# Performance work log

Hardware: AMD Instinct MI355X
Metric: run time of the kernel (lower is better)

## Reference

```python
import jax, jax.numpy as jnp
import numpy as np

N_NODES = 100000
N_EDGES = 1600000
D_IN = 128
D_HID = 128
D_OUT = 16


def gcn_conv(x, W, b, src, dst, deg_inv_sqrt, deg_inv):
    # PyG GCNConv: transform then normalized aggregate with self-loops.
    h = x @ W  # [N, H]
    norm = deg_inv_sqrt[src] * deg_inv_sqrt[dst]  # [E]
    msg = h[src] * norm[:, None]  # [E, H] gather
    agg = jax.ops.segment_sum(msg, dst, num_segments=N_NODES)  # scatter-add
    agg = agg + h * deg_inv[:, None]  # self-loop term (weight deg^-1)
    return agg + b


def setup_inputs() -> dict:
    key = jax.random.key(0)
    ks = jax.random.split(key, 10)
    x = jax.random.normal(ks[0], (N_NODES, D_IN), dtype=jnp.float32)
    edge_index = jax.random.randint(ks[1], (2, N_EDGES), 0, N_NODES)
    s = 1.0 / np.sqrt(D_IN)
    sh = 1.0 / np.sqrt(D_HID)
    W0 = jax.random.uniform(ks[2], (D_IN, D_HID), jnp.float32, -s, s)
    b0 = jnp.zeros((D_HID,), jnp.float32)
    W1 = jax.random.uniform(ks[3], (D_HID, D_HID), jnp.float32, -sh, sh)
    b1 = jnp.zeros((D_HID,), jnp.float32)
    W2 = jax.random.uniform(ks[4], (D_HID, D_HID), jnp.float32, -sh, sh)
    b2 = jnp.zeros((D_HID,), jnp.float32)
    Wr = jax.random.uniform(ks[5], (D_HID, D_OUT), jnp.float32, -sh, sh)
    br = jax.random.uniform(ks[6], (D_OUT,), jnp.float32, -sh, sh)
    return {"x": x, "edge_index": edge_index, "W0": W0, "b0": b0,
            "W1": W1, "b1": b1, "W2": W2, "b2": b2, "Wr": Wr, "br": br}


def reference(x, edge_index, W0, b0, W1, b1, W2, b2, Wr, br):
    src, dst = edge_index[0], edge_index[1]
    # degree with self-loops: deg[i] = 1 + indegree(i)
    deg = jax.ops.segment_sum(jnp.ones((N_EDGES,), x.dtype), dst,
                              num_segments=N_NODES) + 1.0
    deg_inv_sqrt = deg ** -0.5
    deg_inv = 1.0 / deg
    h = x
    for W, b in ((W0, b0), (W1, b1), (W2, b2)):
        h = gcn_conv(h, W, b, src, dst, deg_inv_sqrt, deg_inv)
        h = jax.nn.relu(h)  # dropout is identity at inference
    out = h @ Wr + br
    return jax.nn.sigmoid(out) * 0.8 + 0.1
```

## Files before the change

### kernel.cpp

```cpp
#include <hip/hip_runtime.h>
#include <math.h>

#define N_NODES 100000
#define N_EDGES 1600000
#define NBUCKET 782
#define EB      256
#define EPB     6250

typedef __attribute__((ext_vector_type(8))) __bf16 bf16x8;
typedef __attribute__((ext_vector_type(4))) float  f32x4;


static __device__ __forceinline__ unsigned short f2bf(float f) {
    unsigned int u = __float_as_uint(f);
    unsigned int r = (u + 0x7FFFu + ((u >> 16) & 1u)) >> 16;
    return (unsigned short)r;
}
static __device__ __forceinline__ float bf2f(unsigned short h) {
    return __uint_as_float(((unsigned int)h) << 16);
}

__global__ void wconv_kernel(const float* __restrict__ W, unsigned short* __restrict__ Wt) {
    int n = blockIdx.x;
    int k = threadIdx.x;
    Wt[n * 128 + k] = f2bf(W[k * 128 + n]);
}


__global__ __launch_bounds__(256) void hist_kernel(const int* __restrict__ dst,
                                                   int* __restrict__ hist ) {
    __shared__ int h[NBUCKET];
    int tid = threadIdx.x;
    for (int b = tid; b < NBUCKET; b += 256) h[b] = 0;
    __syncthreads();
    int base = blockIdx.x * EPB;
    for (int i = tid; i < EPB; i += 256)
        atomicAdd(&h[dst[base + i] >> 7], 1);
    __syncthreads();
    int* hrow = hist + (size_t)blockIdx.x * NBUCKET;
    for (int b = tid; b < NBUCKET; b += 256) hrow[b] = h[b];
}

__global__ __launch_bounds__(256) void scan_hist_kernel(const int* __restrict__ hist,
                                                        int* __restrict__ blkoffT,
                                                        int* __restrict__ btotal) {
    __shared__ int s[256];
    int b = blockIdx.x;
    int k = threadIdx.x;
    int v = hist[(size_t)k * NBUCKET + b];
    s[k] = v;
    __syncthreads();
    for (int off = 1; off < 256; off <<= 1) {
        int t = 0;
        if (k >= off) t = s[k - off];
        __syncthreads();
        s[k] += t;
        __syncthreads();
    }
    blkoffT[(size_t)b * 256 + k] = s[k] - v;
    if (k == 255) btotal[b] = s[255];
}

__global__ __launch_bounds__(256) void bucket_scan_kernel(const int* __restrict__ btotal,
                                                          int* __restrict__ bucket_start) {
    __shared__ int cs[256];
    int tid = threadIdx.x;
    int base = tid * 4;
    int v[4];
    int sum = 0;
#pragma unroll
    for (int q = 0; q < 4; q++) {
        int idx = base + q;
        v[q] = (idx < NBUCKET) ? btotal[idx] : 0;
        sum += v[q];
    }
    cs[tid] = sum;
    __syncthreads();
    for (int off = 1; off < 256; off <<= 1) {
        int t = 0;
        if (tid >= off) t = cs[tid - off];
        __syncthreads();
        cs[tid] += t;
        __syncthreads();
    }
    int run = cs[tid] - sum;
#pragma unroll
    for (int q = 0; q < 4; q++) {
        int idx = base + q;
        if (idx < NBUCKET + 1) bucket_start[idx] = run;
        run += v[q];
    }
}

__global__ __launch_bounds__(256) void scatter_kernel(const int* __restrict__ src,
                                                      const int* __restrict__ dst,
                                                      const int* __restrict__ blkoffT,
                                                      const int* __restrict__ bucket_start,
                                                      int* __restrict__ pairs) {
    __shared__ int cur[NBUCKET];
    int tid = threadIdx.x;
    for (int b = tid; b < NBUCKET; b += 256)
        cur[b] = bucket_start[b] + blkoffT[(size_t)b * 256 + blockIdx.x];
    __syncthreads();
    int base = blockIdx.x * EPB;
    for (int i = tid; i < EPB; i += 256) {
        int d = dst[base + i];
        int s = src[base + i];
        int pos = atomicAdd(&cur[d >> 7], 1);
        pairs[pos] = s | ((d & 127) << 20);
    }
}

__global__ __launch_bounds__(256) void build_csr_kernel(const int* __restrict__ pairs,
                                                        const int* __restrict__ bucket_start,
                                                        int* __restrict__ rowstart,
                                                        int* __restrict__ counts,
                                                        float* __restrict__ dis,
                                                        int* __restrict__ csr_src) {
    __shared__ int lcnt[128];
    __shared__ int lsc[128];
    __shared__ int lcur[128];
    int tid = threadIdx.x;
    int b = blockIdx.x;
    int node_base = b * 128;
    if (tid < 128) lcnt[tid] = 0;
    __syncthreads();
    int rs = bucket_start[b];
    int re = bucket_start[b + 1];
    for (int e = rs + tid; e < re; e += 256)
        atomicAdd(&lcnt[pairs[e] >> 20], 1);
    __syncthreads();
    if (tid < 128) lsc[tid] = lcnt[tid];
    __syncthreads();
    for (int off = 1; off < 128; off <<= 1) {
        int t = 0;
        if (tid < 128 && tid >= off) t = lsc[tid - off];
        __syncthreads();
        if (tid < 128) lsc[tid] += t;
        __syncthreads();
    }
    if (tid < 128) {
        int node = node_base + tid;
        if (node < N_NODES) {
            int startg = rs + lsc[tid] - lcnt[tid];
            rowstart[node] = startg;
            counts[node]   = lcnt[tid];
            dis[node]      = rsqrtf((float)(lcnt[tid] + 1));
            lcur[tid]      = startg;
        }
    }
    __syncthreads();
    for (int e = rs + tid; e < re; e += 256) {
        int v = pairs[e];
        int pos = atomicAdd(&lcur[v >> 20], 1);
        csr_src[pos] = v & 0xFFFFF;
    }
}


template <bool FP32IN>
__global__ __launch_bounds__(256) void gemm_mfma_kernel(const void* __restrict__ Xin,
                                                        const unsigned short* __restrict__ Wt,
                                                        const float* __restrict__ dis,
                                                        unsigned short* __restrict__ Yb) {
    int tid = threadIdx.x;
    int rowBase = blockIdx.x * 128;
    int lane = tid & 63;
    int wv_  = tid >> 6;
    int wrow = wv_ * 32;
    int lr   = lane & 15;
    int loct = lane >> 4;

    const float*          Xf = (const float*)Xin;
    const unsigned short* Xb = (const unsigned short*)Xin;

    f32x4 acc[2][8];
#pragma unroll
    for (int a = 0; a < 2; a++)
#pragma unroll
        for (int b = 0; b < 8; b++) acc[a][b] = (f32x4){0.f, 0.f, 0.f, 0.f};

#pragma unroll
    for (int s = 0; s < 4; s++) {
        int kb = s * 32 + loct * 8;
        bf16x8 afr[2];
#pragma unroll
        for (int t2 = 0; t2 < 2; t2++) {
            int row = rowBase + wrow + t2 * 16 + lr;
            if (row < N_NODES) {
                if (FP32IN) {
                    float4 v0 = *(const float4*)&Xf[(size_t)row * 128 + kb];
                    float4 v1 = *(const float4*)&Xf[(size_t)row * 128 + kb + 4];
                    union { unsigned short u[8]; bf16x8 v; } cv;
                    cv.u[0] = f2bf(v0.x); cv.u[1] = f2bf(v0.y);
                    cv.u[2] = f2bf(v0.z); cv.u[3] = f2bf(v0.w);
                    cv.u[4] = f2bf(v1.x); cv.u[5] = f2bf(v1.y);
                    cv.u[6] = f2bf(v1.z); cv.u[7] = f2bf(v1.w);
                    afr[t2] = cv.v;
                } else {
                    afr[t2] = *(const bf16x8*)&Xb[(size_t)row * 128 + kb];
                }
            } else {
                union { unsigned short u[8]; bf16x8 v; } z;
#pragma unroll
                for (int j = 0; j < 8; j++) z.u[j] = 0;
                afr[t2] = z.v;
            }
        }
#pragma unroll
        for (int tc = 0; tc < 8; tc++) {
            int col = tc * 16 + lr;
            bf16x8 bfr = *(const bf16x8*)&Wt[(size_t)col * 128 + kb];
            acc[0][tc] = __builtin_amdgcn_mfma_f32_16x16x32_bf16(afr[0], bfr, acc[0][tc], 0, 0, 0);
            acc[1][tc] = __builtin_amdgcn_mfma_f32_16x16x32_bf16(afr[1], bfr, acc[1][tc], 0, 0, 0);
        }
    }

#pragma unroll
    for (int t2 = 0; t2 < 2; t2++) {
        int rbase = rowBase + wrow + t2 * 16 + (lane >> 4) * 4;
        float sc[4];
#pragma unroll
        for (int r = 0; r < 4; r++)
            sc[r] = (rbase + r < N_NODES) ? dis[rbase + r] : 0.f;
#pragma unroll
        for (int tc = 0; tc < 8; tc++) {
            int col = tc * 16 + lr;
#pragma unroll
            for (int r = 0; r < 4; r++) {
                int row = rbase + r;
                if (row < N_NODES)
                    Yb[(size_t)row * 128 + col] = f2bf(acc[t2][tc][r] * sc[r]);
            }
        }
    }
}


__global__ __launch_bounds__(256) void aggregate_kernel(const unsigned short* __restrict__ Hs,
                                                        const float* __restrict__ dis,
                                                        const int* __restrict__ rowstart,
                                                        const int* __restrict__ counts,
                                                        const int* __restrict__ csr_src,
                                                        const float* __restrict__ bias,
                                                        unsigned int* __restrict__ OutU) {
    int node = blockIdx.x * 4 + (threadIdx.x >> 6);
    node = __builtin_amdgcn_readfirstlane(node);
    int lane = threadIdx.x & 63;
    if (node >= N_NODES) return;
    int c0 = lane * 2;

    unsigned int ow = *(const unsigned int*)&Hs[(size_t)node * 128 + c0];
    float accx = bf2f((unsigned short)(ow & 0xffffu));
    float accy = bf2f((unsigned short)(ow >> 16));

    int start = rowstart[node];
    int cnt   = counts[node];
    int end = start + cnt;
    int j = start;

    for (; j + 7 < end; j += 8) {
        int s0 = __builtin_nontemporal_load(&csr_src[j]);
        int s1 = __builtin_nontemporal_load(&csr_src[j + 1]);
        int s2 = __builtin_nontemporal_load(&csr_src[j + 2]);
        int s3 = __builtin_nontemporal_load(&csr_src[j + 3]);
        int s4 = __builtin_nontemporal_load(&csr_src[j + 4]);
        int s5 = __builtin_nontemporal_load(&csr_src[j + 5]);
        int s6 = __builtin_nontemporal_load(&csr_src[j + 6]);
        int s7 = __builtin_nontemporal_load(&csr_src[j + 7]);
        unsigned int w0 = *(const unsigned int*)&Hs[(size_t)s0 * 128 + c0];
        unsigned int w1 = *(const unsigned int*)&Hs[(size_t)s1 * 128 + c0];
        unsigned int w2 = *(const unsigned int*)&Hs[(size_t)s2 * 128 + c0];
        unsigned int w3 = *(const unsigned int*)&Hs[(size_t)s3 * 128 + c0];
        unsigned int w4 = *(const unsigned int*)&Hs[(size_t)s4 * 128 + c0];
        unsigned int w5 = *(const unsigned int*)&Hs[(size_t)s5 * 128 + c0];
        unsigned int w6 = *(const unsigned int*)&Hs[(size_t)s6 * 128 + c0];
        unsigned int w7 = *(const unsigned int*)&Hs[(size_t)s7 * 128 + c0];
        accx += ((bf2f((unsigned short)(w0 & 0xffffu)) + bf2f((unsigned short)(w1 & 0xffffu)))
               + (bf2f((unsigned short)(w2 & 0xffffu)) + bf2f((unsigned short)(w3 & 0xffffu))))
              + ((bf2f((unsigned short)(w4 & 0xffffu)) + bf2f((unsigned short)(w5 & 0xffffu)))
               + (bf2f((unsigned short)(w6 & 0xffffu)) + bf2f((unsigned short)(w7 & 0xffffu))));
        accy += ((bf2f((unsigned short)(w0 >> 16)) + bf2f((unsigned short)(w1 >> 16)))
               + (bf2f((unsigned short)(w2 >> 16)) + bf2f((unsigned short)(w3 >> 16))))
              + ((bf2f((unsigned short)(w4 >> 16)) + bf2f((unsigned short)(w5 >> 16)))
               + (bf2f((unsigned short)(w6 >> 16)) + bf2f((unsigned short)(w7 >> 16))));
    }
    for (; j + 1 < end; j += 2) {
        int s0 = __builtin_nontemporal_load(&csr_src[j]);
        int s1 = __builtin_nontemporal_load(&csr_src[j + 1]);
        unsigned int w0 = *(const unsigned int*)&Hs[(size_t)s0 * 128 + c0];
        unsigned int w1 = *(const unsigned int*)&Hs[(size_t)s1 * 128 + c0];
        accx += bf2f((unsigned short)(w0 & 0xffffu)) + bf2f((unsigned short)(w1 & 0xffffu));
        accy += bf2f((unsigned short)(w0 >> 16)) + bf2f((unsigned short)(w1 >> 16));
    }
    if (j < end) {
        int s0 = __builtin_nontemporal_load(&csr_src[j]);
        unsigned int w0 = *(const unsigned int*)&Hs[(size_t)s0 * 128 + c0];
        accx += bf2f((unsigned short)(w0 & 0xffffu));
        accy += bf2f((unsigned short)(w0 >> 16));
    }

    float dsi = dis[node];
    float2 bb = *(const float2*)&bias[c0];
    float rx = fmaxf(fmaf(accx, dsi, bb.x), 0.f);
    float ry = fmaxf(fmaf(accy, dsi, bb.y), 0.f);
    unsigned int pk = (unsigned int)f2bf(rx) | ((unsigned int)f2bf(ry) << 16);
    __builtin_nontemporal_store(pk, &OutU[(size_t)node * 64 + lane]);
}


__global__ __launch_bounds__(256) void final_kernel(const unsigned short* __restrict__ Hb,
                                                    const float* __restrict__ Wr,
                                                    const float* __restrict__ br,
                                                    float* __restrict__ out) {
    __shared__ float hs[16][132];
    __shared__ float ws[128][16];
    int tid = threadIdx.x;
    int rowBase = blockIdx.x * 16;
    {
#pragma unroll
        for (int q = 0; q < 4; q++) {
            int idx = q * 256 + tid;
            int r  = idx >> 6;
            int kp = (idx & 63) * 2;
            unsigned int w = *(const unsigned int*)&Hb[(size_t)(rowBase + r) * 128 + kp];
            hs[r][kp]     = bf2f((unsigned short)(w & 0xffffu));
            hs[r][kp + 1] = bf2f((unsigned short)(w >> 16));
        }
#pragma unroll
        for (int q = 0; q < 8; q++) {
            int idx = q * 256 + tid;
            ws[idx >> 4][idx & 15] = Wr[idx];
        }
    }
    __syncthreads();
    int row = tid >> 4;
    int c   = tid & 15;
    float acc = br[c];
#pragma unroll
    for (int k = 0; k < 128; k++)
        acc = fmaf(hs[row][k], ws[k][c], acc);
    int grow = rowBase + row;
    float sg = 1.f / (1.f + expf(-acc));
    out[(size_t)grow * 16 + c] = 0.8f * sg + 0.1f;
}


extern "C" void kernel_launch(void* const* d_in, const int* in_sizes, int n_in,
                              void* d_out, int out_size, void* d_ws, size_t ws_size,
                              hipStream_t stream) {
    const float* x  = (const float*)d_in[0];
    const int*   ei = (const int*)d_in[1];
    const int*   src = ei;
    const int*   dst = ei + N_EDGES;
    const float* W0 = (const float*)d_in[2];
    const float* b0 = (const float*)d_in[3];
    const float* W1 = (const float*)d_in[4];
    const float* b1 = (const float*)d_in[5];
    const float* W2 = (const float*)d_in[6];
    const float* b2 = (const float*)d_in[7];
    const float* Wr = (const float*)d_in[8];
    const float* br = (const float*)d_in[9];
    float* out = (float*)d_out;

    char* ws = (char*)d_ws;
    size_t off = 0;
    auto take = [&](size_t bytes) {
        char* p = ws + off;
        off += (bytes + 255) & ~(size_t)255;
        return p;
    };
    unsigned short* hAb      = (unsigned short*)take((size_t)N_NODES * 128 * 2);
    unsigned short* hBs      = (unsigned short*)take((size_t)N_NODES * 128 * 2);
    unsigned short* Wt       = (unsigned short*)take(128 * 128 * 2);
    int*            counts   = (int*)take((size_t)N_NODES * 4);
    int*            rowstart = (int*)take((size_t)N_NODES * 4);
    float*          dis      = (float*)take((size_t)N_NODES * 4);
    int*            csr_src  = (int*)take((size_t)N_EDGES * 4);
    int*            pairs    = (int*)take((size_t)N_EDGES * 4);
    int*            hist     = (int*)take((size_t)EB * NBUCKET * 4);
    int*            blkoffT  = (int*)take((size_t)NBUCKET * EB * 4);
    int*            btotal   = (int*)take(1024 * 4);
    int*            bstart   = (int*)take(1024 * 4);
    (void)ws_size; (void)in_sizes; (void)n_in; (void)out_size;

    hist_kernel<<<EB, 256, 0, stream>>>(dst, hist);
    scan_hist_kernel<<<NBUCKET, 256, 0, stream>>>(hist, blkoffT, btotal);
    bucket_scan_kernel<<<1, 256, 0, stream>>>(btotal, bstart);
    scatter_kernel<<<EB, 256, 0, stream>>>(src, dst, blkoffT, bstart, pairs);
    build_csr_kernel<<<NBUCKET, 256, 0, stream>>>(pairs, bstart, rowstart, counts, dis, csr_src);

    const float* Wl[3] = {W0, W1, W2};
    const float* bl[3] = {b0, b1, b2};
    int gemmBlocks = (N_NODES + 127) / 128;
    for (int l = 0; l < 3; l++) {
        wconv_kernel<<<128, 128, 0, stream>>>(Wl[l], Wt);
        if (l == 0)
            gemm_mfma_kernel<true><<<gemmBlocks, 256, 0, stream>>>(x, Wt, dis, hBs);
        else
            gemm_mfma_kernel<false><<<gemmBlocks, 256, 0, stream>>>(hAb, Wt, dis, hBs);
        aggregate_kernel<<<N_NODES / 4, 256, 0, stream>>>(hBs, dis, rowstart, counts,
                                                          csr_src, bl[l], (unsigned int*)hAb);
    }
    final_kernel<<<N_NODES / 16, 256, 0, stream>>>(hAb, Wr, br, out);
}
```

Baseline: 470.0 us.

## Batch weight conversion, fold bucket scan into consumers, shrink GEMM row tile

Converts all three weight matrices in one launch instead of one per layer. Removes the single-block bucket_scan kernel by having each scatter and build_csr block redo the small 782-entry scan in LDS. Halves the GEMM rows per block to 64, so each wave handles 16 rows and the grid has more blocks. Together this cuts about four launches and may improve GEMM occupancy, in exchange for redundant scan work per block and fewer MFMAs per weight-fragment load.

```diff
diff --git a/kernel.cpp b/kernel.cpp
--- a/kernel.cpp
+++ b/kernel.cpp
@@ -20,10 +20,14 @@
     return __uint_as_float(((unsigned int)h) << 16);
 }
 
-__global__ void wconv_kernel(const float* __restrict__ W, unsigned short* __restrict__ Wt) {
-    int n = blockIdx.x;
+__global__ void wconv3_kernel(const float* __restrict__ W0, const float* __restrict__ W1,
+                              const float* __restrict__ W2, unsigned short* __restrict__ Wt3) {
+    int b = blockIdx.x;
+    int l = b >> 7;
+    int n = b & 127;
     int k = threadIdx.x;
-    Wt[n * 128 + k] = f2bf(W[k * 128 + n]);
+    const float* W = (l == 0) ? W0 : (l == 1) ? W1 : W2;
+    Wt3[l * 16384 + n * 128 + k] = f2bf(W[k * 128 + n]);
 }
 
 
@@ -61,9 +65,8 @@
     if (k == 255) btotal[b] = s[255];
 }
 
-__global__ __launch_bounds__(256) void bucket_scan_kernel(const int* __restrict__ btotal,
-                                                          int* __restrict__ bucket_start) {
-    __shared__ int cs[256];
+static __device__ __forceinline__ void scan_btotal_lds(const int* __restrict__ btotal,
+                                                       int* bs_l, int* cs) {
     int tid = threadIdx.x;
     int base = tid * 4;
     int v[4];
@@ -87,20 +90,24 @@
 #pragma unroll
     for (int q = 0; q < 4; q++) {
         int idx = base + q;
-        if (idx < NBUCKET + 1) bucket_start[idx] = run;
+        if (idx < NBUCKET + 1) bs_l[idx] = run;
         run += v[q];
     }
+    __syncthreads();
 }
 
 __global__ __launch_bounds__(256) void scatter_kernel(const int* __restrict__ src,
                                                       const int* __restrict__ dst,
                                                       const int* __restrict__ blkoffT,
-                                                      const int* __restrict__ bucket_start,
+                                                      const int* __restrict__ btotal,
                                                       int* __restrict__ pairs) {
     __shared__ int cur[NBUCKET];
-    int tid = threadIdx.x;
+    __shared__ int bs_l[NBUCKET + 2];
+    __shared__ int cs[256];
+    int tid = threadIdx.x;
+    scan_btotal_lds(btotal, bs_l, cs);
     for (int b = tid; b < NBUCKET; b += 256)
-        cur[b] = bucket_start[b] + blkoffT[(size_t)b * 256 + blockIdx.x];
+        cur[b] = bs_l[b] + blkoffT[(size_t)b * 256 + blockIdx.x];
     __syncthreads();
     int base = blockIdx.x * EPB;
     for (int i = tid; i < EPB; i += 256) {
@@ -112,21 +119,24 @@
 }
 
 __global__ __launch_bounds__(256) void build_csr_kernel(const int* __restrict__ pairs,
-                                                        const int* __restrict__ bucket_start,
+                                                        const int* __restrict__ btotal,
                                                         int* __restrict__ rowstart,
                                                         int* __restrict__ counts,
                                                         float* __restrict__ dis,
                                                         int* __restrict__ csr_src) {
+    __shared__ int bs_l[NBUCKET + 2];
+    __shared__ int cs[256];
     __shared__ int lcnt[128];
     __shared__ int lsc[128];
     __shared__ int lcur[128];
     int tid = threadIdx.x;
     int b = blockIdx.x;
     int node_base = b * 128;
+    scan_btotal_lds(btotal, bs_l, cs);
     if (tid < 128) lcnt[tid] = 0;
     __syncthreads();
-    int rs = bucket_start[b];
-    int re = bucket_start[b + 1];
+    int rs = bs_l[b];
+    int re = bs_l[b + 1];
     for (int e = rs + tid; e < re; e += 256)
         atomicAdd(&lcnt[pairs[e] >> 20], 1);
     __syncthreads();
@@ -164,74 +174,65 @@
                                                         const float* __restrict__ dis,
                                                         unsigned short* __restrict__ Yb) {
     int tid = threadIdx.x;
-    int rowBase = blockIdx.x * 128;
+    int rowBase = blockIdx.x * 64;
     int lane = tid & 63;
     int wv_  = tid >> 6;
-    int wrow = wv_ * 32;
     int lr   = lane & 15;
     int loct = lane >> 4;
 
     const float*          Xf = (const float*)Xin;
     const unsigned short* Xb = (const unsigned short*)Xin;
 
-    f32x4 acc[2][8];
-#pragma unroll
-    for (int a = 0; a < 2; a++)
-#pragma unroll
-        for (int b = 0; b < 8; b++) acc[a][b] = (f32x4){0.f, 0.f, 0.f, 0.f};
+    f32x4 acc[8];
+#pragma unroll
+    for (int b = 0; b < 8; b++) acc[b] = (f32x4){0.f, 0.f, 0.f, 0.f};
+
+    int arow = rowBase + wv_ * 16 + lr;
 
 #pragma unroll
     for (int s = 0; s < 4; s++) {
         int kb = s * 32 + loct * 8;
-        bf16x8 afr[2];
-#pragma unroll
-        for (int t2 = 0; t2 < 2; t2++) {
-            int row = rowBase + wrow + t2 * 16 + lr;
-            if (row < N_NODES) {
-                if (FP32IN) {
-                    float4 v0 = *(const float4*)&Xf[(size_t)row * 128 + kb];
-                    float4 v1 = *(const float4*)&Xf[(size_t)row * 128 + kb + 4];
-                    union { unsigned short u[8]; bf16x8 v; } cv;
-                    cv.u[0] = f2bf(v0.x); cv.u[1] = f2bf(v0.y);
-                    cv.u[2] = f2bf(v0.z); cv.u[3] = f2bf(v0.w);
-                    cv.u[4] = f2bf(v1.x); cv.u[5] = f2bf(v1.y);
-                    cv.u[6] = f2bf(v1.z); cv.u[7] = f2bf(v1.w);
-                    afr[t2] = cv.v;
-                } else {
-                    afr[t2] = *(const bf16x8*)&Xb[(size_t)row * 128 + kb];
-                }
+        bf16x8 afr;
+        if (arow < N_NODES) {
+            if (FP32IN) {
+                float4 v0 = *(const float4*)&Xf[(size_t)arow * 128 + kb];
+                float4 v1 = *(const float4*)&Xf[(size_t)arow * 128 + kb + 4];
+                union { unsigned short u[8]; bf16x8 v; } cv;
+                cv.u[0] = f2bf(v0.x); cv.u[1] = f2bf(v0.y);
+                cv.u[2] = f2bf(v0.z); cv.u[3] = f2bf(v0.w);
+                cv.u[4] = f2bf(v1.x); cv.u[5] = f2bf(v1.y);
+                cv.u[6] = f2bf(v1.z); cv.u[7] = f2bf(v1.w);
+                afr = cv.v;
             } else {
-                union { unsigned short u[8]; bf16x8 v; } z;
-#pragma unroll
-                for (int j = 0; j < 8; j++) z.u[j] = 0;
-                afr[t2] = z.v;
+                afr = *(const bf16x8*)&Xb[(size_t)arow * 128 + kb];
             }
+        } else {
+            union { unsigned short u[8]; bf16x8 v; } z;
+#pragma unroll
+            for (int j = 0; j < 8; j++) z.u[j] = 0;
+            afr = z.v;
         }
 #pragma unroll
         for (int tc = 0; tc < 8; tc++) {
             int col = tc * 16 + lr;
             bf16x8 bfr = *(const bf16x8*)&Wt[(size_t)col * 128 + kb];
-            acc[0][tc] = __builtin_amdgcn_mfma_f32_16x16x32_bf16(afr[0], bfr, acc[0][tc], 0, 0, 0);
-            acc[1][tc] = __builtin_amdgcn_mfma_f32_16x16x32_bf16(afr[1], bfr, acc[1][tc], 0, 0, 0);
-        }
-    }
-
-#pragma unroll
-    for (int t2 = 0; t2 < 2; t2++) {
-        int rbase = rowBase + wrow + t2 * 16 + (lane >> 4) * 4;
-        float sc[4];
-#pragma unroll
-        for (int r = 0; r < 4; r++)
-            sc[r] = (rbase + r < N_NODES) ? dis[rbase + r] : 0.f;
-#pragma unroll
-        for (int tc = 0; tc < 8; tc++) {
-            int col = tc * 16 + lr;
-#pragma unroll
-            for (int r = 0; r < 4; r++) {
-                int row = rbase + r;
-                if (row < N_NODES)
-                    Yb[(size_t)row * 128 + col] = f2bf(acc[t2][tc][r] * sc[r]);
-            }
+            acc[tc] = __builtin_amdgcn_mfma_f32_16x16x32_bf16(afr, bfr, acc[tc], 0, 0, 0);
+        }
+    }
+
+    int rbase = rowBase + wv_ * 16 + loct * 4;
+    float sc[4];
+#pragma unroll
+    for (int r = 0; r < 4; r++)
+        sc[r] = (rbase + r < N_NODES) ? dis[rbase + r] : 0.f;
+#pragma unroll
+    for (int tc = 0; tc < 8; tc++) {
+        int col = tc * 16 + lr;
+#pragma unroll
+        for (int r = 0; r < 4; r++) {
+            int row = rbase + r;
+            if (row < N_NODES)
+                Yb[(size_t)row * 128 + col] = f2bf(acc[tc][r] * sc[r]);
         }
     }
 }
@@ -372,7 +373,7 @@
     };
     unsigned short* hAb      = (unsigned short*)take((size_t)N_NODES * 128 * 2);
     unsigned short* hBs      = (unsigned short*)take((size_t)N_NODES * 128 * 2);
-    unsigned short* Wt       = (unsigned short*)take(128 * 128 * 2);
+    unsigned short* Wt3      = (unsigned short*)take(3 * 128 * 128 * 2);
     int*            counts   = (int*)take((size_t)N_NODES * 4);
     int*            rowstart = (int*)take((size_t)N_NODES * 4);
     float*          dis      = (float*)take((size_t)N_NODES * 4);
@@ -381,20 +382,19 @@
     int*            hist     = (int*)take((size_t)EB * NBUCKET * 4);
     int*            blkoffT  = (int*)take((size_t)NBUCKET * EB * 4);
     int*            btotal   = (int*)take(1024 * 4);
-    int*            bstart   = (int*)take(1024 * 4);
     (void)ws_size; (void)in_sizes; (void)n_in; (void)out_size;
+
+    wconv3_kernel<<<384, 128, 0, stream>>>(W0, W1, W2, Wt3);
 
     hist_kernel<<<EB, 256, 0, stream>>>(dst, hist);
     scan_hist_kernel<<<NBUCKET, 256, 0, stream>>>(hist, blkoffT, btotal);
-    bucket_scan_kernel<<<1, 256, 0, stream>>>(btotal, bstart);
-    scatter_kernel<<<EB, 256, 0, stream>>>(src, dst, blkoffT, bstart, pairs);
-    build_csr_kernel<<<NBUCKET, 256, 0, stream>>>(pairs, bstart, rowstart, counts, dis, csr_src);
-
-    const float* Wl[3] = {W0, W1, W2};
+    scatter_kernel<<<EB, 256, 0, stream>>>(src, dst, blkoffT, btotal, pairs);
+    build_csr_kernel<<<NBUCKET, 256, 0, stream>>>(pairs, btotal, rowstart, counts, dis, csr_src);
+
     const float* bl[3] = {b0, b1, b2};
-    int gemmBlocks = (N_NODES + 127) / 128;
+    int gemmBlocks = (N_NODES + 63) / 64;
     for (int l = 0; l < 3; l++) {
-        wconv_kernel<<<128, 128, 0, stream>>>(Wl[l], Wt);
+        const unsigned short* Wt = Wt3 + l * 16384;
         if (l == 0)
             gemm_mfma_kernel<true><<<gemmBlocks, 256, 0, stream>>>(x, Wt, dis, hBs);
         else
```

Result: slower. 485.0 us (+3.2%).
